# Kernel tuning notes

Measured on AMD Instinct MI355X. Metric: run time of the kernel, lower is better.

## Reference

```python
import jax, jax.numpy as jnp
import numpy as np

DIM = 1024
HEADS = 16
HEAD_DIM = DIM // HEADS
SCALE = HEAD_DIM ** -0.5


def setup_inputs() -> dict:
    key = jax.random.key(0)
    ks = jax.random.split(key, 9)
    b, n, m = 4, 1024, 1024
    x = jax.random.normal(ks[0], (b, n, DIM), dtype=jnp.float32)
    context = jax.random.normal(ks[1], (b, m, DIM), dtype=jnp.float32)
    mask = jax.random.randint(ks[2], (b, n, 32, 32), 0, 2, dtype=jnp.int32)
    s = DIM ** -0.5
    Wq = jax.random.normal(ks[3], (DIM, DIM), dtype=jnp.float32) * s
    bq = jnp.zeros((DIM,), dtype=jnp.float32)
    Wkv = jax.random.normal(ks[4], (DIM, 2 * DIM), dtype=jnp.float32) * s
    bkv = jnp.zeros((2 * DIM,), dtype=jnp.float32)
    Wp = jax.random.normal(ks[5], (DIM, DIM), dtype=jnp.float32) * s
    bp = jnp.zeros((DIM,), dtype=jnp.float32)
    return {"x": x, "context": context, "mask": mask,
            "Wq": Wq, "bq": bq, "Wkv": Wkv, "bkv": bkv, "Wp": Wp, "bp": bp}


def reference(x, context, mask, Wq, bq, Wkv, bkv, Wp, bp):
    b, n, _ = x.shape
    m = context.shape[1]
    h, d = HEADS, HEAD_DIM
    # projections
    q = (x @ Wq + bq).reshape(b, n, h, d).transpose(0, 2, 1, 3)       # [b,h,n,d]
    kv = (context @ Wkv + bkv).reshape(b, m, 2, h, d)
    k = kv[:, :, 0].transpose(0, 2, 1, 3)                              # [b,h,m,d]
    v = kv[:, :, 1].transpose(0, 2, 1, 3)                              # [b,h,m,d]
    dots = jnp.einsum('bhnd,bhmd->bhnm', q, k) * SCALE                 # [b,h,n,m]
    # mask: [b,n,H,W] -> [b,1,n,m]; masked_fill where mask == 0
    mflat = mask.reshape(b, n, m)[:, None]                             # [b,1,n,m]
    dots = jnp.where(mflat == 0, -jnp.inf, dots)
    attn = jax.nn.softmax(dots, axis=-1)
    out = jnp.einsum('bhnm,bhmd->bhnd', attn, v)
    out = out.transpose(0, 2, 1, 3).reshape(b, n, h * d)
    return out @ Wp + bp
```

## Files before the change

### kernel.cpp

```cpp
#include <hip/hip_runtime.h>

typedef __bf16 bf16;
typedef __bf16 bf16x8 __attribute__((ext_vector_type(8)));
typedef float f32x4 __attribute__((ext_vector_type(4)));
typedef unsigned long long u64;

#define MFMA16(a, b, c) __builtin_amdgcn_mfma_f32_16x16x32_bf16(a, b, c, 0, 0, 0)

__device__ __forceinline__ void gl_lds16(const void* g, void* l) {
  __builtin_amdgcn_global_load_lds(
      (const __attribute__((address_space(1))) unsigned int*)g,
      (__attribute__((address_space(3))) unsigned int*)l, 16, 0, 0);
}

__global__ __launch_bounds__(256)
void prep_k(const float* __restrict__ Wq, const float* __restrict__ Wkv,
            const float* __restrict__ Wp, const int* __restrict__ mask,
            const float* __restrict__ context, bf16* __restrict__ BqkvT,
            bf16* __restrict__ WpT, u64* __restrict__ maskbits,
            bf16* __restrict__ cb) {
  const int bx = blockIdx.x;
  const int tid = threadIdx.x;
  if (bx >= 1280) {
    const size_t i = ((size_t)(bx - 1280) * 256 + tid) * 8;
    f32x4 a0 = *(const f32x4*)(context + i);
    f32x4 a1 = *(const f32x4*)(context + i + 4);
    bf16x8 t;
#pragma unroll
    for (int j = 0; j < 4; ++j) { t[j] = (bf16)a0[j]; t[4 + j] = (bf16)a1[j]; }
    *(bf16x8*)(cb + i) = t;
    return;
  }
  if (bx >= 1024) {
    const int idx = (bx - 1024) * 256 + tid;
    const int4* p = (const int4*)(mask + (size_t)idx * 64);
    u64 v = 0;
#pragma unroll
    for (int i = 0; i < 16; ++i) {
      int4 m = p[i];
      v |= (u64)(m.x != 0) << (4 * i);
      v |= (u64)(m.y != 0) << (4 * i + 1);
      v |= (u64)(m.z != 0) << (4 * i + 2);
      v |= (u64)(m.w != 0) << (4 * i + 3);
    }
    maskbits[idx] = v;
    return;
  }
  const int ct = bx >> 4, rt = bx & 15;
  const float* src;
  bf16* dst;
  int C, c0, drow0;
  if (ct < 16) {
    src = Wq; C = 1024; c0 = ct * 64; dst = BqkvT; drow0 = c0;
  } else if (ct < 48) {
    src = Wkv; C = 2048; c0 = (ct - 16) * 64; dst = BqkvT; drow0 = 1024 + c0;
  } else {
    src = Wp; C = 1024; c0 = (ct - 48) * 64; dst = WpT; drow0 = c0;
  }
  __shared__ bf16 T[64][72];
  const int r0 = rt * 64;
#pragma unroll
  for (int i = 0; i < 2; ++i) {
    int c = i * 256 + tid;
    int row = c >> 3, col = (c & 7) * 8;
    const float* sp = &src[(size_t)(r0 + row) * C + c0 + col];
    f32x4 a0 = *(const f32x4*)sp;
    f32x4 a1 = *(const f32x4*)(sp + 4);
    bf16x8 t;
#pragma unroll
    for (int j = 0; j < 4; ++j) { t[j] = (bf16)a0[j]; t[4 + j] = (bf16)a1[j]; }
    *(bf16x8*)&T[row][col] = t;
  }
  __syncthreads();
#pragma unroll
  for (int i = 0; i < 2; ++i) {
    int c = i * 256 + tid;
    int orow = c >> 3, ocol = (c & 7) * 8;
    bf16x8 v;
#pragma unroll
    for (int j = 0; j < 8; ++j) v[j] = T[ocol + j][orow];
    *(bf16x8*)&dst[(size_t)(drow0 + orow) * 1024 + r0 + ocol] = v;
  }
}

template <int EPI>
__global__ __launch_bounds__(256)
void gemm_db(const float* __restrict__ Af0, const float* __restrict__ Af1,
             const bf16* __restrict__ Ab, const bf16* __restrict__ Bt,
             const float* __restrict__ bias0, const float* __restrict__ bias1,
             bf16* __restrict__ oq, bf16* __restrict__ ok,
             bf16* __restrict__ ovt, float* __restrict__ outf) {
  __shared__ bf16 As[2][64][64];
  __shared__ bf16 Bs[2][128][64];
  const int tid = threadIdx.x;
  const int lane = tid & 63;
  const int w = tid >> 6;
  const int wm = (w >> 1) * 32, wn = (w & 1) * 64;
  const int l15 = lane & 15, l4 = lane >> 4;
  const int lrow = lane >> 3;
  const int scol = ((lane & 7) ^ (lrow & 7)) * 8;
  const int m0 = blockIdx.x * 64;
  const int n0 = blockIdx.y * 128;

  const bool a_async = (EPI == 0) || (n0 >= 1024);
  const float* Af = (EPI == 1) ? ((n0 < 1024) ? Af0 : Af1) : nullptr;
  const bf16* Asrc = (EPI == 0) ? Ab : ((const bf16*)Af1);

  const int ar = tid >> 2;
  const int acb = (tid & 3) * 2;

  f32x4 pf[4];
  f32x4 acc[2][4] = {};

#define STAGE_B(kk, buf)                                                      \
  _Pragma("unroll") for (int it = 0; it < 4; ++it) {                          \
    const int r = w * 32 + it * 8;                                            \
    gl_lds16(&Bt[(size_t)(n0 + r + lrow) * 1024 + (kk) + scol],               \
             &Bs[buf][r][0]);                                                 \
  }
#define STAGE_A_ASYNC(kk, buf)                                                \
  _Pragma("unroll") for (int it = 0; it < 2; ++it) {                          \
    const int r = w * 16 + it * 8;                                            \
    gl_lds16(&Asrc[(size_t)(m0 + r + lrow) * 1024 + (kk) + scol],             \
             &As[buf][r][0]);                                                 \
  }
#define LOAD_A_F32(kk)                                                        \
  {                                                                           \
    const float* ap = &Af[(size_t)(m0 + ar) * 1024 + (kk) + acb * 8];         \
    pf[0] = *(const f32x4*)ap;                                                \
    pf[1] = *(const f32x4*)(ap + 4);                                          \
    pf[2] = *(const f32x4*)(ap + 8);                                          \
    pf[3] = *(const f32x4*)(ap + 12);                                         \
  }
#define COMMIT_A_F32(buf)                                                     \
  _Pragma("unroll") for (int j = 0; j < 2; ++j) {                             \
    bf16x8 t;                                                                 \
    _Pragma("unroll") for (int u = 0; u < 4; ++u) {                           \
      t[u] = (bf16)pf[2 * j][u];                                              \
      t[4 + u] = (bf16)pf[2 * j + 1][u];                                      \
    }                                                                         \
    *(bf16x8*)&As[buf][ar][((acb + j) ^ (ar & 7)) * 8] = t;                   \
  }

  STAGE_B(0, 0);
  if (a_async) {
    STAGE_A_ASYNC(0, 0);
  } else {
    LOAD_A_F32(0);
    COMMIT_A_F32(0);
  }

  for (int k = 0; k < 16; ++k) {
    const int cur = k & 1, nxt = cur ^ 1;
    if (!a_async && k < 15) LOAD_A_F32((k + 1) * 64);
    __syncthreads();
    if (k < 15) {
      STAGE_B((k + 1) * 64, nxt);
      if (a_async) STAGE_A_ASYNC((k + 1) * 64, nxt);
    }
#pragma unroll
    for (int ks = 0; ks < 2; ++ks) {
      const int sw = ((ks * 4 + l4) ^ (l15 & 7)) * 8;
      bf16x8 af[2], bfr[4];
#pragma unroll
      for (int i = 0; i < 2; ++i)
        af[i] = *(const bf16x8*)&As[cur][wm + i * 16 + l15][sw];
#pragma unroll
      for (int j = 0; j < 4; ++j)
        bfr[j] = *(const bf16x8*)&Bs[cur][wn + j * 16 + l15][sw];
#pragma unroll
      for (int i = 0; i < 2; ++i)
#pragma unroll
        for (int j = 0; j < 4; ++j)
          acc[i][j] = MFMA16(af[i], bfr[j], acc[i][j]);
    }
    if (!a_async && k < 15) COMMIT_A_F32(nxt);
  }

  const float SCALE2 = 0.18033688011112042f;
#pragma unroll
  for (int j = 0; j < 4; ++j) {
    const int col = n0 + wn + j * 16 + l15;
    float bc;
    if (EPI == 1) bc = (col < 1024) ? bias0[col] : bias1[col - 1024];
    else bc = bias0[col];
#pragma unroll
    for (int i = 0; i < 2; ++i) {
#pragma unroll
      for (int r = 0; r < 4; ++r) {
        const int row = m0 + wm + i * 16 + l4 * 4 + r;
        const float v = acc[i][j][r] + bc;
        if (EPI == 0) {
          outf[(size_t)row * 1024 + col] = v;
        } else {
          const int b = row >> 10, n = row & 1023;
          if (col < 1024) {
            const int h = col >> 6, d = col & 63;
            oq[(((size_t)(b * 16 + h)) * 1024 + n) * 64 + d] =
                (bf16)(v * SCALE2);
          } else {
            const int ckv = col - 1024;
            const int s = ckv >> 10, c2 = ckv & 1023;
            const int h = c2 >> 6, d = c2 & 63;
            if (s == 0)
              ok[(((size_t)(b * 16 + h)) * 1024 + n) * 64 + d] = (bf16)v;
            else
              ovt[(((size_t)(b * 16 + h)) * 64 + d) * 1024 + n] = (bf16)v;
          }
        }
      }
    }
  }
#undef STAGE_B
#undef STAGE_A_ASYNC
#undef LOAD_A_F32
#undef COMMIT_A_F32
}

__global__ __launch_bounds__(256)
void attn_kernel(const bf16* __restrict__ q, const bf16* __restrict__ k,
                 const bf16* __restrict__ vT, const u64* __restrict__ maskbits,
                 bf16* __restrict__ ao) {
  const int bh = blockIdx.x;
  const int ntile = blockIdx.y;
  const int b = bh >> 4, h = bh & 15;
  const int tid = threadIdx.x;
  const int lane = tid & 63;
  const int w = tid >> 6;
  const int l15 = lane & 15, l4 = lane >> 4;

  __shared__ bf16 Ks[64][72];
  __shared__ bf16 Vts[64][72];
  __shared__ bf16 Pw[4][16][72];

  const size_t base = (size_t)bh * 65536;
  const int nrow0 = ntile * 64 + w * 16;

  bf16x8 qf[2];
#pragma unroll
  for (int ks = 0; ks < 2; ++ks)
    qf[ks] =
        *(const bf16x8*)&q[base + (size_t)(nrow0 + l15) * 64 + ks * 32 + l4 * 8];

  f32x4 o[4] = {};
  float lsum[4] = {0.0f, 0.0f, 0.0f, 0.0f};

  const u64* mb = maskbits + (size_t)(b * 1024 + nrow0) * 16;

  for (int mt = 0; mt < 16; ++mt) {
#pragma unroll
    for (int i = 0; i < 2; ++i) {
      int c = i * 256 + tid;
      int row = c >> 3, col = (c & 7) * 8;
      *(bf16x8*)&Ks[row][col] =
          *(const bf16x8*)&k[base + (size_t)(mt * 64 + row) * 64 + col];
      *(bf16x8*)&Vts[row][col] =
          *(const bf16x8*)&vT[base + (size_t)row * 1024 + mt * 64 + col];
    }
    __syncthreads();

    f32x4 s[4];
#pragma unroll
    for (int sub = 0; sub < 4; ++sub) s[sub] = f32x4{-12.f, -12.f, -12.f, -12.f};
#pragma unroll
    for (int ks = 0; ks < 2; ++ks) {
#pragma unroll
      for (int sub = 0; sub < 4; ++sub) {
        bf16x8 bfr = *(const bf16x8*)&Ks[sub * 16 + l15][ks * 32 + l4 * 8];
        s[sub] = MFMA16(qf[ks], bfr, s[sub]);
      }
    }

    u64 wbits[4];
#pragma unroll
    for (int r = 0; r < 4; ++r) wbits[r] = mb[(size_t)(l4 * 4 + r) * 16 + mt];

#pragma unroll
    for (int sub = 0; sub < 4; ++sub) {
#pragma unroll
      for (int r = 0; r < 4; ++r) {
        float p = exp2f(s[sub][r]);
        p = ((wbits[r] >> (sub * 16 + l15)) & 1) ? p : 0.0f;
        lsum[r] += p;
        Pw[w][l4 * 4 + r][sub * 16 + l15] = (bf16)p;
      }
    }

#pragma unroll
    for (int ks = 0; ks < 2; ++ks) {
      bf16x8 af = *(const bf16x8*)&Pw[w][l15][ks * 32 + l4 * 8];
#pragma unroll
      for (int sub = 0; sub < 4; ++sub) {
        bf16x8 bfr = *(const bf16x8*)&Vts[sub * 16 + l15][ks * 32 + l4 * 8];
        o[sub] = MFMA16(af, bfr, o[sub]);
      }
    }
    __syncthreads();
  }

  float inv[4];
#pragma unroll
  for (int r = 0; r < 4; ++r) {
    float t = lsum[r];
#pragma unroll
    for (int d = 1; d < 16; d <<= 1) t += __shfl_xor(t, d);
    inv[r] = 1.0f / t;
  }

#pragma unroll
  for (int sub = 0; sub < 4; ++sub) {
#pragma unroll
    for (int r = 0; r < 4; ++r) {
      const int n = nrow0 + l4 * 4 + r;
      const size_t idx =
          ((size_t)(b * 1024 + n)) * 1024 + h * 64 + sub * 16 + l15;
      ao[idx] = (bf16)(o[sub][r] * inv[r]);
    }
  }
}

extern "C" void kernel_launch(void* const* d_in, const int* in_sizes, int n_in,
                              void* d_out, int out_size, void* d_ws,
                              size_t ws_size, hipStream_t stream) {
  const float* x = (const float*)d_in[0];
  const float* context = (const float*)d_in[1];
  const int* mask = (const int*)d_in[2];
  const float* Wq = (const float*)d_in[3];
  const float* bq = (const float*)d_in[4];
  const float* Wkv = (const float*)d_in[5];
  const float* bkv = (const float*)d_in[6];
  const float* Wp = (const float*)d_in[7];
  const float* bp = (const float*)d_in[8];
  float* out = (float*)d_out;

  char* ws = (char*)d_ws;
  bf16* cb = (bf16*)(ws);
  bf16* aow = (bf16*)(ws);
  bf16* BqkvT = (bf16*)(ws + (8ull << 20));
  bf16* qw = (bf16*)(ws + (14ull << 20));
  bf16* kw = (bf16*)(ws + (22ull << 20));
  bf16* vtw = (bf16*)(ws + (30ull << 20));
  u64* maskbits = (u64*)(ws + (38ull << 20));
  bf16* WpT = (bf16*)(ws + (38ull << 20) + (512ull << 10));

  const dim3 blk(256);

  prep_k<<<dim3(3328), blk, 0, stream>>>(Wq, Wkv, Wp, mask, context, BqkvT,
                                         WpT, maskbits, cb);

  gemm_db<1><<<dim3(64, 24), blk, 0, stream>>>(x, (const float*)cb, nullptr,
                                               BqkvT, bq, bkv, qw, kw, vtw,
                                               nullptr);

  attn_kernel<<<dim3(64, 16), blk, 0, stream>>>(qw, kw, vtw, maskbits, aow);

  gemm_db<0><<<dim3(64, 8), blk, 0, stream>>>(nullptr, nullptr, aow, WpT, bp,
                                              nullptr, nullptr, nullptr,
                                              nullptr, out);
}
```

Measured before the change: 231.9 us.

## Pre-convert x to bf16 and switch GEMMs to larger single-buffered tiles

x is now converted to bf16 in the prep kernel, so the QKV GEMM loads every A operand through async global-to-LDS copies instead of converting fp32 inline. The double-buffered 64x128 GEMM is replaced by a single-buffered kernel with 128-row tiles and a templated N width: 128 for the QKV projection and 64 for the output projection. The larger tiles raise per-wave MFMA reuse. In exchange, load/compute overlap from double buffering is lost, an extra sync is added per k-step, and there is an extra pass over x in memory.

```diff
diff --git a/kernel.cpp b/kernel.cpp
--- a/kernel.cpp
+++ b/kernel.cpp
@@ -16,11 +16,22 @@
 __global__ __launch_bounds__(256)
 void prep_k(const float* __restrict__ Wq, const float* __restrict__ Wkv,
             const float* __restrict__ Wp, const int* __restrict__ mask,
-            const float* __restrict__ context, bf16* __restrict__ BqkvT,
-            bf16* __restrict__ WpT, u64* __restrict__ maskbits,
-            bf16* __restrict__ cb) {
+            const float* __restrict__ context, const float* __restrict__ x,
+            bf16* __restrict__ BqkvT, bf16* __restrict__ WpT,
+            u64* __restrict__ maskbits, bf16* __restrict__ cb,
+            bf16* __restrict__ xb) {
   const int bx = blockIdx.x;
   const int tid = threadIdx.x;
+  if (bx >= 3328) {
+    const size_t i = ((size_t)(bx - 3328) * 256 + tid) * 8;
+    f32x4 a0 = *(const f32x4*)(x + i);
+    f32x4 a1 = *(const f32x4*)(x + i + 4);
+    bf16x8 t;
+#pragma unroll
+    for (int j = 0; j < 4; ++j) { t[j] = (bf16)a0[j]; t[4 + j] = (bf16)a1[j]; }
+    *(bf16x8*)(xb + i) = t;
+    return;
+  }
   if (bx >= 1280) {
     const size_t i = ((size_t)(bx - 1280) * 256 + tid) * 8;
     f32x4 a0 = *(const f32x4*)(context + i);
@@ -83,109 +94,72 @@
   }
 }
 
-template <int EPI>
+template <int EPI, int BN>
 __global__ __launch_bounds__(256)
-void gemm_db(const float* __restrict__ Af0, const float* __restrict__ Af1,
-             const bf16* __restrict__ Ab, const bf16* __restrict__ Bt,
-             const float* __restrict__ bias0, const float* __restrict__ bias1,
-             bf16* __restrict__ oq, bf16* __restrict__ ok,
-             bf16* __restrict__ ovt, float* __restrict__ outf) {
-  __shared__ bf16 As[2][64][64];
-  __shared__ bf16 Bs[2][128][64];
+void gemm_sb(const bf16* __restrict__ A0, const bf16* __restrict__ A1,
+             const bf16* __restrict__ Bt, const float* __restrict__ bias0,
+             const float* __restrict__ bias1, bf16* __restrict__ oq,
+             bf16* __restrict__ ok, bf16* __restrict__ ovt,
+             float* __restrict__ outf) {
+  constexpr int NJ = BN / 32;
+  __shared__ bf16 As[128][64];
+  __shared__ bf16 Bs[BN][64];
   const int tid = threadIdx.x;
   const int lane = tid & 63;
   const int w = tid >> 6;
-  const int wm = (w >> 1) * 32, wn = (w & 1) * 64;
+  const int wm = (w >> 1) * 64;
+  const int wn = (w & 1) * (BN / 2);
   const int l15 = lane & 15, l4 = lane >> 4;
   const int lrow = lane >> 3;
   const int scol = ((lane & 7) ^ (lrow & 7)) * 8;
-  const int m0 = blockIdx.x * 64;
-  const int n0 = blockIdx.y * 128;
-
-  const bool a_async = (EPI == 0) || (n0 >= 1024);
-  const float* Af = (EPI == 1) ? ((n0 < 1024) ? Af0 : Af1) : nullptr;
-  const bf16* Asrc = (EPI == 0) ? Ab : ((const bf16*)Af1);
-
-  const int ar = tid >> 2;
-  const int acb = (tid & 3) * 2;
-
-  f32x4 pf[4];
-  f32x4 acc[2][4] = {};
-
-#define STAGE_B(kk, buf)                                                      \
-  _Pragma("unroll") for (int it = 0; it < 4; ++it) {                          \
-    const int r = w * 32 + it * 8;                                            \
-    gl_lds16(&Bt[(size_t)(n0 + r + lrow) * 1024 + (kk) + scol],               \
-             &Bs[buf][r][0]);                                                 \
-  }
-#define STAGE_A_ASYNC(kk, buf)                                                \
-  _Pragma("unroll") for (int it = 0; it < 2; ++it) {                          \
-    const int r = w * 16 + it * 8;                                            \
-    gl_lds16(&Asrc[(size_t)(m0 + r + lrow) * 1024 + (kk) + scol],             \
-             &As[buf][r][0]);                                                 \
-  }
-#define LOAD_A_F32(kk)                                                        \
-  {                                                                           \
-    const float* ap = &Af[(size_t)(m0 + ar) * 1024 + (kk) + acb * 8];         \
-    pf[0] = *(const f32x4*)ap;                                                \
-    pf[1] = *(const f32x4*)(ap + 4);                                          \
-    pf[2] = *(const f32x4*)(ap + 8);                                          \
-    pf[3] = *(const f32x4*)(ap + 12);                                         \
-  }
-#define COMMIT_A_F32(buf)                                                     \
-  _Pragma("unroll") for (int j = 0; j < 2; ++j) {                             \
-    bf16x8 t;                                                                 \
-    _Pragma("unroll") for (int u = 0; u < 4; ++u) {                           \
-      t[u] = (bf16)pf[2 * j][u];                                              \
-      t[4 + u] = (bf16)pf[2 * j + 1][u];                                      \
-    }                                                                         \
-    *(bf16x8*)&As[buf][ar][((acb + j) ^ (ar & 7)) * 8] = t;                   \
-  }
-
-  STAGE_B(0, 0);
-  if (a_async) {
-    STAGE_A_ASYNC(0, 0);
-  } else {
-    LOAD_A_F32(0);
-    COMMIT_A_F32(0);
-  }
+  const int m0 = blockIdx.x * 128;
+  const int n0 = blockIdx.y * BN;
+
+  const bf16* Asrc = (EPI == 1) ? ((n0 < 1024) ? A0 : A1) : A0;
+
+  f32x4 acc[4][NJ] = {};
 
   for (int k = 0; k < 16; ++k) {
-    const int cur = k & 1, nxt = cur ^ 1;
-    if (!a_async && k < 15) LOAD_A_F32((k + 1) * 64);
+    const int kk = k * 64;
+#pragma unroll
+    for (int it = 0; it < 4; ++it) {
+      const int r = w * 32 + it * 8;
+      gl_lds16(&Asrc[(size_t)(m0 + r + lrow) * 1024 + kk + scol], &As[r][0]);
+    }
+#pragma unroll
+    for (int it = 0; it < BN / 32; ++it) {
+      const int r = w * (BN / 4) + it * 8;
+      gl_lds16(&Bt[(size_t)(n0 + r + lrow) * 1024 + kk + scol], &Bs[r][0]);
+    }
     __syncthreads();
-    if (k < 15) {
-      STAGE_B((k + 1) * 64, nxt);
-      if (a_async) STAGE_A_ASYNC((k + 1) * 64, nxt);
-    }
 #pragma unroll
     for (int ks = 0; ks < 2; ++ks) {
       const int sw = ((ks * 4 + l4) ^ (l15 & 7)) * 8;
-      bf16x8 af[2], bfr[4];
-#pragma unroll
-      for (int i = 0; i < 2; ++i)
-        af[i] = *(const bf16x8*)&As[cur][wm + i * 16 + l15][sw];
-#pragma unroll
-      for (int j = 0; j < 4; ++j)
-        bfr[j] = *(const bf16x8*)&Bs[cur][wn + j * 16 + l15][sw];
-#pragma unroll
-      for (int i = 0; i < 2; ++i)
-#pragma unroll
-        for (int j = 0; j < 4; ++j)
+      bf16x8 af[4], bfr[NJ];
+#pragma unroll
+      for (int i = 0; i < 4; ++i)
+        af[i] = *(const bf16x8*)&As[wm + i * 16 + l15][sw];
+#pragma unroll
+      for (int j = 0; j < NJ; ++j)
+        bfr[j] = *(const bf16x8*)&Bs[wn + j * 16 + l15][sw];
+#pragma unroll
+      for (int i = 0; i < 4; ++i)
+#pragma unroll
+        for (int j = 0; j < NJ; ++j)
           acc[i][j] = MFMA16(af[i], bfr[j], acc[i][j]);
     }
-    if (!a_async && k < 15) COMMIT_A_F32(nxt);
+    __syncthreads();
   }
 
   const float SCALE2 = 0.18033688011112042f;
 #pragma unroll
-  for (int j = 0; j < 4; ++j) {
+  for (int j = 0; j < NJ; ++j) {
     const int col = n0 + wn + j * 16 + l15;
     float bc;
     if (EPI == 1) bc = (col < 1024) ? bias0[col] : bias1[col - 1024];
     else bc = bias0[col];
 #pragma unroll
-    for (int i = 0; i < 2; ++i) {
+    for (int i = 0; i < 4; ++i) {
 #pragma unroll
       for (int r = 0; r < 4; ++r) {
         const int row = m0 + wm + i * 16 + l4 * 4 + r;
@@ -211,10 +185,6 @@
       }
     }
   }
-#undef STAGE_B
-#undef STAGE_A_ASYNC
-#undef LOAD_A_F32
-#undef COMMIT_A_F32
 }
 
 __global__ __launch_bounds__(256)
@@ -336,25 +306,25 @@
   char* ws = (char*)d_ws;
   bf16* cb = (bf16*)(ws);
   bf16* aow = (bf16*)(ws);
-  bf16* BqkvT = (bf16*)(ws + (8ull << 20));
-  bf16* qw = (bf16*)(ws + (14ull << 20));
-  bf16* kw = (bf16*)(ws + (22ull << 20));
-  bf16* vtw = (bf16*)(ws + (30ull << 20));
-  u64* maskbits = (u64*)(ws + (38ull << 20));
-  bf16* WpT = (bf16*)(ws + (38ull << 20) + (512ull << 10));
+  bf16* xb = (bf16*)(ws + (8ull << 20));
+  bf16* BqkvT = (bf16*)(ws + (16ull << 20));
+  bf16* qw = (bf16*)(ws + (22ull << 20));
+  bf16* kw = (bf16*)(ws + (30ull << 20));
+  bf16* vtw = (bf16*)(ws + (38ull << 20));
+  u64* maskbits = (u64*)(ws + (46ull << 20));
+  bf16* WpT = (bf16*)(ws + (46ull << 20) + (512ull << 10));
 
   const dim3 blk(256);
 
-  prep_k<<<dim3(3328), blk, 0, stream>>>(Wq, Wkv, Wp, mask, context, BqkvT,
-                                         WpT, maskbits, cb);
-
-  gemm_db<1><<<dim3(64, 24), blk, 0, stream>>>(x, (const float*)cb, nullptr,
-                                               BqkvT, bq, bkv, qw, kw, vtw,
-                                               nullptr);
+  prep_k<<<dim3(5376), blk, 0, stream>>>(Wq, Wkv, Wp, mask, context, x, BqkvT,
+                                         WpT, maskbits, cb, xb);
+
+  gemm_sb<1, 128><<<dim3(32, 24), blk, 0, stream>>>(xb, cb, BqkvT, bq, bkv,
+                                                    qw, kw, vtw, nullptr);
 
   attn_kernel<<<dim3(64, 16), blk, 0, stream>>>(qw, kw, vtw, maskbits, aow);
 
-  gemm_db<0><<<dim3(64, 8), blk, 0, stream>>>(nullptr, nullptr, aow, WpT, bp,
-                                              nullptr, nullptr, nullptr,
-                                              nullptr, out);
-}
+  gemm_sb<0, 64><<<dim3(32, 16), blk, 0, stream>>>(aow, nullptr, WpT, bp,
+                                                   nullptr, nullptr, nullptr,
+                                                   nullptr, out);
+}
```

New measurement: 219.2 us. -5.5%, faster.
